# Kernel tuning notes

Hardware: AMD Instinct MI355X
Metric: run time of the kernel (lower is better)

The kernel has to match this reference:

```python
import jax, jax.numpy as jnp
import numpy as np

N_NODES = 10000
N_EDGES = 160000
N_GRAPHS = 64
TOWERS = 5
F_IN = 75        # divide_input=False -> each tower sees full 75-dim input
F_OUT = 15       # 75 // 5 towers
N_LAYERS = 4
POST_IN = (4 * 3 + 1) * F_IN  # (aggregators*scalers + 1) * F_in = 975
AVG_DEG_LOG = float(np.log(17.0))  # avg_deg['log'] from the deg histogram (avg degree 16)
BN_EPS = 1e-5


def setup_inputs() -> dict:
    key = jax.random.key(0)
    ks = jax.random.split(key, 20)
    g = lambda k, shape, s=0.05: (jax.random.normal(k, shape, jnp.float32) * s)
    inp = {}
    inp["x"] = jax.random.normal(ks[0], (N_NODES, 2), jnp.float32)
    inp["edge_index"] = jax.random.randint(ks[1], (2, N_EDGES), 0, N_NODES)
    inp["batch"] = jnp.sort(jax.random.randint(ks[2], (N_NODES,), 0, N_GRAPHS))
    # pre_lin: Linear(2, 75)
    inp["pre_lin_W"] = g(ks[3], (2, 75));   inp["pre_lin_b"] = g(ks[4], (75,))
    # 4 PNAConv layers, params stacked over layers
    inp["pre_W"]  = g(ks[5], (N_LAYERS, TOWERS, 2 * F_IN, F_IN))   # per-tower pre-MLP Linear(150,75)
    inp["pre_b"]  = g(ks[6], (N_LAYERS, TOWERS, F_IN))
    inp["post_W"] = g(ks[7], (N_LAYERS, TOWERS, POST_IN, F_OUT))   # per-tower post-MLP Linear(975,15)
    inp["post_b"] = g(ks[8], (N_LAYERS, TOWERS, F_OUT))
    inp["lin_W"]  = g(ks[9], (N_LAYERS, 75, 75))                    # mixing Linear(75,75)
    inp["lin_b"]  = g(ks[10], (N_LAYERS, 75))
    inp["bn_scale"] = jnp.ones((N_LAYERS, 75), jnp.float32) + g(ks[11], (N_LAYERS, 75))
    inp["bn_bias"]  = g(ks[12], (N_LAYERS, 75))
    # head MLP: 75 -> 50 -> 25 -> 1
    inp["mlp_W1"] = g(ks[13], (75, 50)); inp["mlp_b1"] = g(ks[14], (50,))
    inp["mlp_W2"] = g(ks[15], (50, 25)); inp["mlp_b2"] = g(ks[16], (25,))
    inp["mlp_W3"] = g(ks[17], (25, 1));  inp["mlp_b3"] = g(ks[18], (1,))
    return inp


def _pna_layer(h, src, dst, preW, preb, postW, postb, linW, linb, n):
    # message: concat(x_i, x_j) = concat(x[dst], x[src]), per-tower pre-MLP (pre_layers=1)
    e = jnp.concatenate([h[dst], h[src]], axis=-1)                    # [E, 150]
    m = jnp.einsum('ec,tcf->etf', e, preW) + preb                     # [E, T, 75]
    # multi-aggregate at dst: mean, min, max, std
    cnt = jax.ops.segment_sum(jnp.ones((m.shape[0],), m.dtype), dst, n)  # [N]
    d = jnp.maximum(cnt, 1.0)[:, None, None]                          # clamped degree
    mean = jax.ops.segment_sum(m, dst, n) / d
    mean_sq = jax.ops.segment_sum(m * m, dst, n) / d
    std = jnp.sqrt(jax.nn.relu(mean_sq - mean * mean) + 1e-5)
    empty = (cnt == 0)[:, None, None]
    mn = jnp.where(empty, 0.0, jax.ops.segment_min(m, dst, n))
    mx = jnp.where(empty, 0.0, jax.ops.segment_max(m, dst, n))
    agg = jnp.concatenate([mean, mn, mx, std], axis=-1)               # [N, T, 300]
    # scalers: identity, amplification, attenuation
    logd = jnp.log(d + 1.0)
    out = jnp.concatenate([agg, agg * (logd / AVG_DEG_LOG), agg * (AVG_DEG_LOG / logd)], axis=-1)  # [N, T, 900]
    # concat tower input, per-tower post-MLP, concat towers, final lin
    xt = jnp.broadcast_to(h[:, None, :], (n, TOWERS, F_IN))
    out = jnp.concatenate([xt, out], axis=-1)                         # [N, T, 975]
    out = jnp.einsum('ntc,tcf->ntf', out, postW) + postb              # [N, T, 15]
    out = out.reshape(n, TOWERS * F_OUT)                              # [N, 75]
    return out @ linW + linb


def reference(x, edge_index, batch, pre_lin_W, pre_lin_b, pre_W, pre_b,
              post_W, post_b, lin_W, lin_b, bn_scale, bn_bias,
              mlp_W1, mlp_b1, mlp_W2, mlp_b2, mlp_W3, mlp_b3):
    n = x.shape[0]
    src, dst = edge_index[0], edge_index[1]
    h = x @ pre_lin_W + pre_lin_b
    for l in range(N_LAYERS):
        out = _pna_layer(h, src, dst, pre_W[l], pre_b[l], post_W[l], post_b[l],
                         lin_W[l], lin_b[l], n)
        # BatchNorm1d (training-mode batch stats, biased variance) + ReLU
        mu = out.mean(axis=0)
        var = out.var(axis=0)
        h = jax.nn.relu((out - mu) / jnp.sqrt(var + BN_EPS) * bn_scale[l] + bn_bias[l])
    pooled = jax.ops.segment_sum(h, batch, N_GRAPHS)                  # global_add_pool [G, 75]
    z = jax.nn.relu(pooled @ mlp_W1 + mlp_b1)
    z = jax.nn.relu(z @ mlp_W2 + mlp_b2)
    return z @ mlp_W3 + mlp_b3                                        # [G, 1]
```

## Files before the change

### kernel.cpp

```cpp
#include <hip/hip_runtime.h>

#define NN 10000
#define NE 160000
#define NG 64
#define NT 5
#define NF 75
#define NL 4
#define LOG17 2.8332133f
#define ROWB 384
#define ASTR 328
#define A1STR 104
#define NCT 56

typedef __attribute__((ext_vector_type(8))) short short8v;
typedef __attribute__((ext_vector_type(4))) float float4v;

__device__ __forceinline__ unsigned short f2bf(float x){
  unsigned u = __float_as_uint(x);
  unsigned r = (u + 0x7FFFu + ((u >> 16) & 1u)) >> 16;
  return (unsigned short)r;
}
__device__ __forceinline__ float blo(unsigned u){ return __uint_as_float(u << 16); }
__device__ __forceinline__ float bhi(unsigned u){ return __uint_as_float(u & 0xFFFF0000u); }

__device__ __forceinline__ int swzk(int k){
  int ks = k >> 5, r = k & 31;
  return (ks << 5) | (((r & 15) >> 2) << 3) | ((r >> 4) << 2) | (r & 3);
}
__device__ __forceinline__ short8v ld8(const unsigned short* p){
  union { uint4 u; short8v v; } x;
  x.u = *(const uint4*)p;
  return x.v;
}

__global__ __launch_bounds__(256) void k_init_h(const float* __restrict__ x,
    const float* __restrict__ W, const float* __restrict__ b, float* __restrict__ h){
  int i = blockIdx.x*256 + threadIdx.x;
  if (i >= NN*NF) return;
  int n = i / NF, f = i - n*NF;
  h[i] = x[2*n]*W[f] + x[2*n+1]*W[NF+f] + b[f];
}

__global__ __launch_bounds__(256) void k_count(const int* __restrict__ ei, int* __restrict__ cnt){
  int e = blockIdx.x*256 + threadIdx.x;
  if (e < NE) atomicAdd(&cnt[ei[NE + e]], 1);
}

__global__ __launch_bounds__(1024) void k_scan(const int* __restrict__ cnt,
    int* __restrict__ off, int* __restrict__ cur){
  __shared__ int buf[1024];
  __shared__ int carry;
  int tid = threadIdx.x;
  if (tid == 0) carry = 0;
  __syncthreads();
  for (int base = 0; base < NN; base += 1024){
    int i = base + tid;
    int v = (i < NN) ? cnt[i] : 0;
    buf[tid] = v;
    __syncthreads();
    for (int d = 1; d < 1024; d <<= 1){
      int t = (tid >= d) ? buf[tid - d] : 0;
      __syncthreads();
      buf[tid] += t;
      __syncthreads();
    }
    int c = carry;
    if (i < NN){ int ex = c + buf[tid] - v; off[i] = ex; cur[i] = ex; }
    int tot = buf[1023];
    __syncthreads();
    if (tid == 0) carry = c + tot;
    __syncthreads();
  }
  if (tid == 0) off[NN] = NE;
}

__global__ __launch_bounds__(256) void k_scatter(const int* __restrict__ ei,
    int* __restrict__ cur, int* __restrict__ csr){
  int e = blockIdx.x*256 + threadIdx.x;
  if (e < NE){
    int d = ei[NE + e];
    int p = atomicAdd(&cur[d], 1);
    csr[p] = ei[e];
  }
}

__global__ __launch_bounds__(256) void k_buildWgS(const float* __restrict__ preW,
    const float* __restrict__ postW, unsigned short* __restrict__ WgS){
  const int TOT = NL*NCT*2*16*96;
  int idx = blockIdx.x*256 + threadIdx.x;
  if (idx >= TOT) return;
  int kpos = idx % 96;
  int rem = idx / 96;
  int n = rem & 15; rem >>= 4;
  int p = rem & 1;  rem >>= 1;
  int ct = rem % NCT;
  int l = rem / NCT;
  int ks = kpos >> 5, r = kpos & 31;
  int b = (r >> 3) & 3, half = (r >> 2) & 1, j = r & 3;
  int k = ks*32 + half*16 + b*4 + j;
  int col = ct*16 + n;
  float val = 0.f;
  if (k < 75){
    if (col < 375){
      int t = col/75, f = col - t*75;
      val = preW[((size_t)(l*NT + t)*150 + 75 + k)*75 + f];
    } else if (col >= 384 && col < 759){
      int jj = col - 384; int t = jj/75, f = jj - t*75;
      val = preW[((size_t)(l*NT + t)*150 + k)*75 + f];
    } else if (col >= 768 && col < 843){
      int jj = col - 768; int t = jj/15, f2 = jj - t*15;
      val = postW[((size_t)(l*NT + t)*975 + k)*15 + f2];
    }
  }
  unsigned short hi = f2bf(val);
  unsigned short outv = hi;
  if (p){
    float rsd = val - __uint_as_float(((unsigned)hi) << 16);
    outv = f2bf(rsd);
  }
  WgS[idx] = outv;
}

__global__ __launch_bounds__(256) void k_buildW45S(const float* __restrict__ postW,
    unsigned short* __restrict__ W45S){
  int idx = blockIdx.x*256 + threadIdx.x;
  const int TOT = NL*NT*3*2*16*320;
  if (idx >= TOT) return;
  int kpos = idx % 320;
  int rem = idx / 320;
  int n = rem & 15; rem >>= 4;
  int p = rem & 1;  rem >>= 1;
  int g = rem % 3;  rem /= 3;
  int t = rem % 5;
  int l = rem / 5;
  int ks = kpos >> 5, r = kpos & 31;
  int b = (r >> 3) & 3, half = (r >> 2) & 1, j = r & 3;
  int k = ks*32 + half*16 + b*4 + j;
  float val = 0.f;
  if (n < 15 && k < 300)
    val = postW[((size_t)(l*NT + t)*975 + 75 + g*300 + k)*15 + n];
  unsigned short hi = f2bf(val);
  unsigned short out = hi;
  if (p){
    float rsd = val - __uint_as_float(((unsigned)hi) << 16);
    out = f2bf(rsd);
  }
  W45S[idx] = out;
}

__global__ __launch_bounds__(256) void k_gemm1(const float* __restrict__ src,
    const unsigned short* __restrict__ WgS, const float* __restrict__ preb,
    const float* __restrict__ bnSp, const float* __restrict__ sc,
    const float* __restrict__ bb, int use_bn,
    unsigned short* __restrict__ out1b, float* __restrict__ baseb,
    float* __restrict__ z, int l){
  __shared__ unsigned short Ah[64*A1STR];
  __shared__ unsigned short Al[64*A1STR];
  int tid = threadIdx.x;
  int bid = blockIdx.x;
  int cg = bid / 157, nt = bid - cg*157;
  int n0 = nt*64;

  for (int i = tid; i < 64*A1STR/2; i += 256){
    ((unsigned*)Ah)[i] = 0; ((unsigned*)Al)[i] = 0;
  }
  __syncthreads();
  for (int idx = tid; idx < 64*75; idx += 256){
    int i = idx/75, c = idx - i*75;
    float v = (n0 + i < NN) ? src[(size_t)n0*75 + idx] : 0.f;
    if (use_bn){
      float mu = bnSp[c] * (1.f/NN);
      float var = bnSp[80 + c] * (1.f/NN) - mu*mu;
      v = fmaxf((v - mu) / sqrtf(var + 1e-5f) * sc[c] + bb[c], 0.f);
    }
    unsigned short hi = f2bf(v);
    float rsd = v - __uint_as_float(((unsigned)hi) << 16);
    int p = i*A1STR + swzk(c);
    Ah[p] = hi; Al[p] = f2bf(rsd);
  }
  __syncthreads();

  int w = tid >> 6, lane = tid & 63;
  int bq = lane >> 4, low = lane & 15;
  const unsigned short* ah = &Ah[(w*16 + low)*A1STR];
  const unsigned short* al = &Al[(w*16 + low)*A1STR];

  float4v acc[8];
  #pragma unroll
  for (int ct = 0; ct < 8; ++ct) acc[ct] = (float4v){0.f,0.f,0.f,0.f};

  #pragma unroll
  for (int ks = 0; ks < 3; ++ks){
    int o = ks*32 + bq*8;
    short8v a_h = ld8(ah + o);
    short8v a_l = ld8(al + o);
    #pragma unroll
    for (int ct = 0; ct < 8; ++ct){
      int gct = cg*8 + ct;
      const unsigned short* wbase = WgS + (((size_t)l*NCT + gct)*2)*16*96 + low*96 + o;
      short8v b_h = ld8(wbase);
      short8v b_l = ld8(wbase + 16*96);
      acc[ct] = __builtin_amdgcn_mfma_f32_16x16x32_bf16(a_h, b_h, acc[ct], 0, 0, 0);
      acc[ct] = __builtin_amdgcn_mfma_f32_16x16x32_bf16(a_h, b_l, acc[ct], 0, 0, 0);
      acc[ct] = __builtin_amdgcn_mfma_f32_16x16x32_bf16(a_l, b_h, acc[ct], 0, 0, 0);
    }
  }

  #pragma unroll
  for (int ct = 0; ct < 8; ++ct){
    int col = cg*128 + ct*16 + low;
    #pragma unroll
    for (int i = 0; i < 4; ++i){
      int n = n0 + w*16 + bq*4 + i;
      if (n < NN){
        float v = acc[ct][i];
        if (col < 375){
          out1b[(size_t)n*ROWB + col] = f2bf(v);
        } else if (col >= 384 && col < 759){
          baseb[(size_t)n*376 + (col - 384)] = v + preb[l*375 + (col - 384)];
        } else if (col >= 768 && col < 843){
          z[(size_t)n*75 + (col - 768)] = v;
        }
      }
    }
  }
}

__device__ __forceinline__ uint4 pack8(const float* v){
  uint4 r;
  r.x = (unsigned)f2bf(v[0]) | ((unsigned)f2bf(v[1]) << 16);
  r.y = (unsigned)f2bf(v[2]) | ((unsigned)f2bf(v[3]) << 16);
  r.z = (unsigned)f2bf(v[4]) | ((unsigned)f2bf(v[5]) << 16);
  r.w = (unsigned)f2bf(v[6]) | ((unsigned)f2bf(v[7]) << 16);
  return r;
}

__global__ __launch_bounds__(256) void k_gather(
    const unsigned short* __restrict__ out1b, const float* __restrict__ baseb,
    const int* __restrict__ off, const int* __restrict__ csr,
    unsigned short* __restrict__ agg){
  int gid = blockIdx.x*256 + threadIdx.x;
  int n = gid >> 6;
  int lane = gid & 63;
  if (n >= NN || lane >= 47) return;
  int fo = lane*8;
  float s[8], ss[8], mn[8], mx[8];
  #pragma unroll
  for (int j = 0; j < 8; ++j){ s[j]=0.f; ss[j]=0.f; mn[j]=3.4e38f; mx[j]=-3.4e38f; }
  int e0 = off[n], e1 = off[n+1], deg = e1 - e0;

#define STT(v,J){ float _v=(v); s[J]+=_v; ss[J]+=_v*_v; mn[J]=fminf(mn[J],_v); mx[J]=fmaxf(mx[J],_v); }
#define PR(X){ STT(blo((X).x),0) STT(bhi((X).x),1) STT(blo((X).y),2) STT(bhi((X).y),3) \
               STT(blo((X).z),4) STT(bhi((X).z),5) STT(blo((X).w),6) STT(bhi((X).w),7) }
  int k = e0;
  for (; k + 4 <= e1; k += 4){
    uint4 a  = *(const uint4*)(out1b + (size_t)csr[k]  *ROWB + fo);
    uint4 b  = *(const uint4*)(out1b + (size_t)csr[k+1]*ROWB + fo);
    uint4 c  = *(const uint4*)(out1b + (size_t)csr[k+2]*ROWB + fo);
    uint4 d2 = *(const uint4*)(out1b + (size_t)csr[k+3]*ROWB + fo);
    PR(a) PR(b) PR(c) PR(d2)
  }
  for (; k < e1; ++k){
    uint4 a = *(const uint4*)(out1b + (size_t)csr[k]*ROWB + fo);
    PR(a)
  }
#undef PR
#undef STT

  float mean[8], sd[8];
  if (deg > 0){
    float rd = 1.f/(float)deg;
    float4 b0 = *(const float4*)(baseb + (size_t)n*376 + fo);
    float4 b1 = *(const float4*)(baseb + (size_t)n*376 + fo + 4);
    float bs[8] = {b0.x,b0.y,b0.z,b0.w,b1.x,b1.y,b1.z,b1.w};
    #pragma unroll
    for (int j = 0; j < 8; ++j){
      float mb = s[j]*rd;
      float var = ss[j]*rd - mb*mb;
      mean[j] = bs[j] + mb;
      sd[j]   = sqrtf(fmaxf(var, 0.f) + 1e-5f);
      mn[j]   = bs[j] + mn[j];
      mx[j]   = bs[j] + mx[j];
    }
  } else {
    #pragma unroll
    for (int j = 0; j < 8; ++j){ mean[j]=0.f; mn[j]=0.f; mx[j]=0.f; sd[j]=sqrtf(1e-5f); }
  }
  unsigned short* ap = agg + (size_t)n*1504 + fo;
  *(uint4*)(ap)        = pack8(mean);
  *(uint4*)(ap + 376)  = pack8(mn);
  *(uint4*)(ap + 752)  = pack8(mx);
  *(uint4*)(ap + 1128) = pack8(sd);
}

__global__ __launch_bounds__(128) void k_post(
    const unsigned short* __restrict__ agg, float* __restrict__ z,
    const int* __restrict__ off, const unsigned short* __restrict__ W45S,
    const float* __restrict__ postb, int l){
  __shared__ unsigned short As[32*ASTR];
  __shared__ float ampl[32], attl[32];
  int tid = threadIdx.x;
  int bid = blockIdx.x;
  const int NTILE = (NN + 31)/32;
  int t = bid / NTILE, nt = bid - t*NTILE;
  int n0 = nt*32;
  if (tid < 32){
    int n = n0 + tid;
    int dd = (n < NN) ? (off[n+1] - off[n]) : 1;
    float d = (float)(dd > 0 ? dd : 1);
    float logd = logf(d + 1.f);
    ampl[tid] = logd*(1.f/LOG17);
    attl[tid] = LOG17/logd;
  }
  for (int idx = tid; idx < 32*320; idx += 128){
    int nl = idx/320, c = idx - nl*320;
    int n = n0 + nl;
    unsigned short raw = 0;
    if (n < NN && c < 300){
      int st = c/75, u = c - st*75;
      raw = agg[(size_t)n*1504 + st*376 + t*75 + u];
    }
    As[nl*ASTR + swzk(c)] = raw;
  }
  __syncthreads();

  int w = tid >> 6, lane = tid & 63;
  int bq = lane >> 4, low = lane & 15;
  const unsigned short* ab = &As[(w*16 + low)*ASTR];
  const unsigned short* wb = W45S + (size_t)((l*NT + t)*3)*2*16*320;
  const unsigned short* b0h = wb + (size_t)(0*2+0)*16*320 + low*320;
  const unsigned short* b0l = wb + (size_t)(0*2+1)*16*320 + low*320;
  const unsigned short* b1h = wb + (size_t)(1*2+0)*16*320 + low*320;
  const unsigned short* b1l = wb + (size_t)(1*2+1)*16*320 + low*320;
  const unsigned short* b2h = wb + (size_t)(2*2+0)*16*320 + low*320;
  const unsigned short* b2l = wb + (size_t)(2*2+1)*16*320 + low*320;

  float4v acc0 = {0.f,0.f,0.f,0.f};
  float4v acc1 = {0.f,0.f,0.f,0.f};
  float4v acc2 = {0.f,0.f,0.f,0.f};
  for (int ks = 0; ks < 10; ++ks){
    int o = ks*32 + bq*8;
    short8v a = ld8(ab + o);
    acc0 = __builtin_amdgcn_mfma_f32_16x16x32_bf16(a, ld8(b0h + o), acc0, 0, 0, 0);
    acc1 = __builtin_amdgcn_mfma_f32_16x16x32_bf16(a, ld8(b1h + o), acc1, 0, 0, 0);
    acc2 = __builtin_amdgcn_mfma_f32_16x16x32_bf16(a, ld8(b2h + o), acc2, 0, 0, 0);
    acc0 = __builtin_amdgcn_mfma_f32_16x16x32_bf16(a, ld8(b0l + o), acc0, 0, 0, 0);
    acc1 = __builtin_amdgcn_mfma_f32_16x16x32_bf16(a, ld8(b1l + o), acc1, 0, 0, 0);
    acc2 = __builtin_amdgcn_mfma_f32_16x16x32_bf16(a, ld8(b2l + o), acc2, 0, 0, 0);
  }

  if (low < 15){
    float pb = postb[(l*NT + t)*15 + low];
    #pragma unroll
    for (int i = 0; i < 4; ++i){
      int m = bq*4 + i;
      int node = n0 + w*16 + m;
      if (node < NN){
        float val = acc0[i] + ampl[w*16 + m]*acc1[i] + attl[w*16 + m]*acc2[i] + pb;
        z[(size_t)node*75 + t*15 + low] += val;
      }
    }
  }
}

__global__ __launch_bounds__(256) void k_lin(const float* __restrict__ z,
    const float* __restrict__ linW, const float* __restrict__ linb,
    float* __restrict__ out2, float* __restrict__ bnS1, int l){
  __shared__ float zs[75][68];
  __shared__ float lw[75][80];
  int tid = threadIdx.x;
  int n0 = blockIdx.x*64;
  for (int idx = tid; idx < 64*75; idx += 256){
    int i = idx/75, c = idx - i*75;
    zs[c][i] = (n0 + i < NN) ? z[(size_t)n0*75 + idx] : 0.f;
  }
  for (int idx = tid; idx < 75*80; idx += 256){
    int c = idx/80, o = idx - c*80;
    lw[c][o] = (o < 75) ? linW[(size_t)l*5625 + c*75 + o] : 0.f;
  }
  __syncthreads();
  int og = tid >> 4, n4 = tid & 15;
  int o0 = og*5;
  float acc[4][5];
  #pragma unroll
  for (int i = 0; i < 4; ++i)
    #pragma unroll
    for (int k = 0; k < 5; ++k) acc[i][k] = 0.f;
  for (int c = 0; c < 75; ++c){
    float4 a = *reinterpret_cast<const float4*>(&zs[c][n4*4]);
    float av[4] = {a.x, a.y, a.z, a.w};
    float wv[5];
    #pragma unroll
    for (int k = 0; k < 5; ++k) wv[k] = lw[c][o0 + k];
    #pragma unroll
    for (int i = 0; i < 4; ++i)
      #pragma unroll
      for (int k = 0; k < 5; ++k) acc[i][k] += av[i]*wv[k];
  }
  float s1p[5], s2p[5];
  #pragma unroll
  for (int k = 0; k < 5; ++k){ s1p[k] = 0.f; s2p[k] = 0.f; }
  #pragma unroll
  for (int i = 0; i < 4; ++i){
    int n = n0 + n4*4 + i;
    if (n >= NN) continue;
    #pragma unroll
    for (int k = 0; k < 5; ++k){
      int o = o0 + k;
      if (o < 75){
        float v = acc[i][k] + linb[l*75 + o];
        out2[(size_t)n*75 + o] = v;
        s1p[k] += v; s2p[k] += v*v;
      }
    }
  }
  __syncthreads();
  float* red = &zs[0][0];
  #pragma unroll
  for (int k = 0; k < 5; ++k){
    int o = o0 + k;
    if (o < 75){ red[o*16 + n4] = s1p[k]; red[1200 + o*16 + n4] = s2p[k]; }
  }
  __syncthreads();
  if (tid < 75){
    float a1 = 0.f, a2 = 0.f;
    #pragma unroll
    for (int j = 0; j < 16; ++j){ a1 += red[tid*16 + j]; a2 += red[1200 + tid*16 + j]; }
    atomicAdd(&bnS1[tid], a1);
    atomicAdd(&bnS1[80 + tid], a2);
  }
}

__global__ __launch_bounds__(256) void k_bnpool(const float* __restrict__ out2,
    const float* __restrict__ bnSp, const float* __restrict__ sc,
    const float* __restrict__ bb, const int* __restrict__ batch,
    float* __restrict__ pooled){
  int i = blockIdx.x*256 + threadIdx.x;
  if (i >= NN*75) return;
  int n = i / 75, f = i - n*75;
  float mu = bnSp[f] * (1.f/NN);
  float var = bnSp[80 + f] * (1.f/NN) - mu*mu;
  float v = fmaxf((out2[i] - mu) / sqrtf(var + 1e-5f) * sc[f] + bb[f], 0.f);
  atomicAdd(&pooled[batch[n]*75 + f], v);
}

__global__ __launch_bounds__(256) void k_head(const float* __restrict__ pooled,
    const float* __restrict__ W1, const float* __restrict__ b1,
    const float* __restrict__ W2, const float* __restrict__ b2,
    const float* __restrict__ W3, const float* __restrict__ b3,
    float* __restrict__ out){
  __shared__ float pl[64*75];
  __shared__ float w1[75*50];
  __shared__ float z1[64*50];
  __shared__ float w2[50*25];
  __shared__ float z2[64*25];
  __shared__ float w3[25];
  __shared__ float bb1[50], bb2[25];
  int tid = threadIdx.x;
  for (int i = tid; i < 64*75; i += 256) pl[i] = pooled[i];
  for (int i = tid; i < 75*50; i += 256) w1[i] = W1[i];
  for (int i = tid; i < 50*25; i += 256) w2[i] = W2[i];
  if (tid < 25) w3[tid] = W3[tid];
  if (tid < 50) bb1[tid] = b1[tid];
  if (tid < 25) bb2[tid] = b2[tid];
  __syncthreads();
  for (int o = tid; o < 64*50; o += 256){
    int g = o / 50, j = o - g*50;
    float acc = bb1[j];
    for (int c = 0; c < 75; ++c) acc += pl[g*75 + c] * w1[c*50 + j];
    z1[o] = fmaxf(acc, 0.f);
  }
  __syncthreads();
  for (int o = tid; o < 64*25; o += 256){
    int g = o / 25, j = o - g*25;
    float acc = bb2[j];
    for (int c = 0; c < 50; ++c) acc += z1[g*50 + c] * w2[c*25 + j];
    z2[o] = fmaxf(acc, 0.f);
  }
  __syncthreads();
  if (tid < 64){
    float acc = b3[0];
    for (int c = 0; c < 25; ++c) acc += z2[tid*25 + c] * w3[c];
    out[tid] = acc;
  }
}

extern "C" void kernel_launch(void* const* d_in, const int* in_sizes, int n_in,
                              void* d_out, int out_size, void* d_ws, size_t ws_size,
                              hipStream_t stream){
  const float* x     = (const float*)d_in[0];
  const int*   ei    = (const int*)  d_in[1];
  const int*   batch = (const int*)  d_in[2];
  const float* plW   = (const float*)d_in[3];
  const float* plb   = (const float*)d_in[4];
  const float* preW  = (const float*)d_in[5];
  const float* preb  = (const float*)d_in[6];
  const float* postW = (const float*)d_in[7];
  const float* postb = (const float*)d_in[8];
  const float* linW  = (const float*)d_in[9];
  const float* linb  = (const float*)d_in[10];
  const float* bns   = (const float*)d_in[11];
  const float* bnb   = (const float*)d_in[12];
  const float* W1    = (const float*)d_in[13];
  const float* b1    = (const float*)d_in[14];
  const float* W2    = (const float*)d_in[15];
  const float* b2    = (const float*)d_in[16];
  const float* W3    = (const float*)d_in[17];
  const float* b3    = (const float*)d_in[18];
  float* out = (float*)d_out;

  float* out2v = (float*)d_ws;
  float* zv    = out2v + 750000;
  float* baseb = zv + 750000;
  unsigned short* W45S = (unsigned short*)(baseb + (size_t)NN*376);
  unsigned short* WgS  = W45S + (size_t)NL*NT*3*2*16*320;
  float* pooled= (float*)(WgS + (size_t)NL*NCT*2*16*96);
  float* bnS   = pooled + 4800;
  unsigned short* out1b = (unsigned short*)(bnS + NL*160);
  unsigned short* aggb  = out1b + (size_t)NN*ROWB;
  float* h0 = (float*)(aggb + (size_t)NN*1504) - 750000;
  int* cnt = (int*)(aggb + (size_t)NN*1504);
  int* off = cnt + NN;
  int* cur = off + NN + 1;
  int* csr = cur + NN;

  hipMemsetAsync(cnt, 0, NN*sizeof(int), stream);
  hipMemsetAsync(bnS, 0, NL*160*sizeof(float), stream);
  hipMemsetAsync(pooled, 0, 4800*sizeof(float), stream);
  hipMemsetAsync(out1b, 0, (size_t)NN*ROWB*sizeof(unsigned short), stream);
  k_init_h<<<(NN*NF + 255)/256, 256, 0, stream>>>(x, plW, plb, h0);
  k_count<<<(NE + 255)/256, 256, 0, stream>>>(ei, cnt);
  k_scan<<<1, 1024, 0, stream>>>(cnt, off, cur);
  k_scatter<<<(NE + 255)/256, 256, 0, stream>>>(ei, cur, csr);
  k_buildWgS<<<(NL*NCT*2*16*96 + 255)/256, 256, 0, stream>>>(preW, postW, WgS);
  k_buildW45S<<<(NL*NT*3*2*16*320 + 255)/256, 256, 0, stream>>>(postW, W45S);

  const int NTILE = (NN + 31)/32;

  for (int l = 0; l < NL; ++l){
    const float* src = (l == 0) ? h0 : out2v;
    const float* bnSp = bnS + (l > 0 ? (l-1)*160 : 0);
    const float* sc = bns + (l > 0 ? (l-1)*75 : 0);
    const float* bb = bnb + (l > 0 ? (l-1)*75 : 0);
    k_gemm1<<<7*157, 256, 0, stream>>>(src, WgS, preb, bnSp, sc, bb, (l > 0),
                                       out1b, baseb, zv, l);
    k_gather<<<(NN*64)/256, 256, 0, stream>>>(out1b, baseb, off, csr, aggb);
    k_post<<<NT*NTILE, 128, 0, stream>>>(aggb, zv, off, W45S, postb, l);
    k_lin<<<157, 256, 0, stream>>>(zv, linW, linb, out2v, bnS + l*160, l);
  }

  k_bnpool<<<(NN*NF + 255)/256, 256, 0, stream>>>(out2v, bnS + 3*160,
                                                  bns + 3*75, bnb + 3*75, batch, pooled);
  k_head<<<1, 256, 0, stream>>>(pooled, W1, b1, W2, b2, W3, b3, out);
}
```

Measured before the change: 655.7 us.

## Pad per-tower features to 80 and write MFMA-swizzled aggregates directly

Rows of out1b and baseb are re-laid out so each tower's 75 features sit in an 80-wide padded slot. The gather kernel now writes the mean/min/max/std aggregates straight into the swizzled per-tower K layout that the post GEMM consumes. This lets k_post load A fragments directly from global memory instead of staging them through shared memory with scalar gathers. The cost is slightly more padded memory and gather threads, and the post weights are rebuilt to match the padded K indexing.

```diff
diff --git a/kernel.cpp b/kernel.cpp
--- a/kernel.cpp
+++ b/kernel.cpp
@@ -7,8 +7,7 @@
 #define NF 75
 #define NL 4
 #define LOG17 2.8332133f
-#define ROWB 384
-#define ASTR 328
+#define ROWP 400
 #define A1STR 104
 #define NCT 56
 
@@ -135,10 +134,11 @@
   int l = rem / 5;
   int ks = kpos >> 5, r = kpos & 31;
   int b = (r >> 3) & 3, half = (r >> 2) & 1, j = r & 3;
-  int k = ks*32 + half*16 + b*4 + j;
+  int kp = ks*32 + half*16 + b*4 + j;
+  int stat = kp / 80, u = kp - stat*80;
   float val = 0.f;
-  if (n < 15 && k < 300)
-    val = postW[((size_t)(l*NT + t)*975 + 75 + g*300 + k)*15 + n];
+  if (n < 15 && u < 75)
+    val = postW[((size_t)(l*NT + t)*975 + 75 + g*300 + stat*75 + u)*15 + n];
   unsigned short hi = f2bf(val);
   unsigned short out = hi;
   if (p){
@@ -215,9 +215,11 @@
       if (n < NN){
         float v = acc[ct][i];
         if (col < 375){
-          out1b[(size_t)n*ROWB + col] = f2bf(v);
+          int t = col/75, u = col - t*75;
+          out1b[(size_t)n*ROWP + t*80 + u] = f2bf(v);
         } else if (col >= 384 && col < 759){
-          baseb[(size_t)n*376 + (col - 384)] = v + preb[l*375 + (col - 384)];
+          int f = col - 384; int t = f/75, u = f - t*75;
+          baseb[(size_t)n*ROWP + t*80 + u] = v + preb[l*375 + f];
         } else if (col >= 768 && col < 843){
           z[(size_t)n*75 + (col - 768)] = v;
         }
@@ -226,12 +228,10 @@
   }
 }
 
-__device__ __forceinline__ uint4 pack8(const float* v){
-  uint4 r;
+__device__ __forceinline__ uint2 pack4(const float* v){
+  uint2 r;
   r.x = (unsigned)f2bf(v[0]) | ((unsigned)f2bf(v[1]) << 16);
   r.y = (unsigned)f2bf(v[2]) | ((unsigned)f2bf(v[3]) << 16);
-  r.z = (unsigned)f2bf(v[4]) | ((unsigned)f2bf(v[5]) << 16);
-  r.w = (unsigned)f2bf(v[6]) | ((unsigned)f2bf(v[7]) << 16);
   return r;
 }
 
@@ -242,8 +242,9 @@
   int gid = blockIdx.x*256 + threadIdx.x;
   int n = gid >> 6;
   int lane = gid & 63;
-  if (n >= NN || lane >= 47) return;
-  int fo = lane*8;
+  if (n >= NN || lane >= 50) return;
+  int p = lane*8;
+  int t = p/80, u0 = p - t*80;
   float s[8], ss[8], mn[8], mx[8];
   #pragma unroll
   for (int j = 0; j < 8; ++j){ s[j]=0.f; ss[j]=0.f; mn[j]=3.4e38f; mx[j]=-3.4e38f; }
@@ -254,14 +255,14 @@
                STT(blo((X).z),4) STT(bhi((X).z),5) STT(blo((X).w),6) STT(bhi((X).w),7) }
   int k = e0;
   for (; k + 4 <= e1; k += 4){
-    uint4 a  = *(const uint4*)(out1b + (size_t)csr[k]  *ROWB + fo);
-    uint4 b  = *(const uint4*)(out1b + (size_t)csr[k+1]*ROWB + fo);
-    uint4 c  = *(const uint4*)(out1b + (size_t)csr[k+2]*ROWB + fo);
-    uint4 d2 = *(const uint4*)(out1b + (size_t)csr[k+3]*ROWB + fo);
+    uint4 a  = *(const uint4*)(out1b + (size_t)csr[k]  *ROWP + p);
+    uint4 b  = *(const uint4*)(out1b + (size_t)csr[k+1]*ROWP + p);
+    uint4 c  = *(const uint4*)(out1b + (size_t)csr[k+2]*ROWP + p);
+    uint4 d2 = *(const uint4*)(out1b + (size_t)csr[k+3]*ROWP + p);
     PR(a) PR(b) PR(c) PR(d2)
   }
   for (; k < e1; ++k){
-    uint4 a = *(const uint4*)(out1b + (size_t)csr[k]*ROWB + fo);
+    uint4 a = *(const uint4*)(out1b + (size_t)csr[k]*ROWP + p);
     PR(a)
   }
 #undef PR
@@ -270,8 +271,8 @@
   float mean[8], sd[8];
   if (deg > 0){
     float rd = 1.f/(float)deg;
-    float4 b0 = *(const float4*)(baseb + (size_t)n*376 + fo);
-    float4 b1 = *(const float4*)(baseb + (size_t)n*376 + fo + 4);
+    float4 b0 = *(const float4*)(baseb + (size_t)n*ROWP + p);
+    float4 b1 = *(const float4*)(baseb + (size_t)n*ROWP + p + 4);
     float bs[8] = {b0.x,b0.y,b0.z,b0.w,b1.x,b1.y,b1.z,b1.w};
     #pragma unroll
     for (int j = 0; j < 8; ++j){
@@ -286,18 +287,25 @@
     #pragma unroll
     for (int j = 0; j < 8; ++j){ mean[j]=0.f; mn[j]=0.f; mx[j]=0.f; sd[j]=sqrtf(1e-5f); }
   }
-  unsigned short* ap = agg + (size_t)n*1504 + fo;
-  *(uint4*)(ap)        = pack8(mean);
-  *(uint4*)(ap + 376)  = pack8(mn);
-  *(uint4*)(ap + 752)  = pack8(mx);
-  *(uint4*)(ap + 1128) = pack8(sd);
+  #pragma unroll
+  for (int j = 0; j < 8; ++j){
+    if (u0 + j >= 75){ mean[j]=0.f; mn[j]=0.f; mx[j]=0.f; sd[j]=0.f; }
+  }
+  unsigned short* ap = agg + (size_t)n*1600 + t*320;
+  *(uint2*)(ap + swzk(0*80 + u0))     = pack4(mean);
+  *(uint2*)(ap + swzk(0*80 + u0 + 4)) = pack4(mean + 4);
+  *(uint2*)(ap + swzk(1*80 + u0))     = pack4(mn);
+  *(uint2*)(ap + swzk(1*80 + u0 + 4)) = pack4(mn + 4);
+  *(uint2*)(ap + swzk(2*80 + u0))     = pack4(mx);
+  *(uint2*)(ap + swzk(2*80 + u0 + 4)) = pack4(mx + 4);
+  *(uint2*)(ap + swzk(3*80 + u0))     = pack4(sd);
+  *(uint2*)(ap + swzk(3*80 + u0 + 4)) = pack4(sd + 4);
 }
 
 __global__ __launch_bounds__(128) void k_post(
     const unsigned short* __restrict__ agg, float* __restrict__ z,
     const int* __restrict__ off, const unsigned short* __restrict__ W45S,
     const float* __restrict__ postb, int l){
-  __shared__ unsigned short As[32*ASTR];
   __shared__ float ampl[32], attl[32];
   int tid = threadIdx.x;
   int bid = blockIdx.x;
@@ -312,21 +320,13 @@
     ampl[tid] = logd*(1.f/LOG17);
     attl[tid] = LOG17/logd;
   }
-  for (int idx = tid; idx < 32*320; idx += 128){
-    int nl = idx/320, c = idx - nl*320;
-    int n = n0 + nl;
-    unsigned short raw = 0;
-    if (n < NN && c < 300){
-      int st = c/75, u = c - st*75;
-      raw = agg[(size_t)n*1504 + st*376 + t*75 + u];
-    }
-    As[nl*ASTR + swzk(c)] = raw;
-  }
   __syncthreads();
 
   int w = tid >> 6, lane = tid & 63;
   int bq = lane >> 4, low = lane & 15;
-  const unsigned short* ab = &As[(w*16 + low)*ASTR];
+  int node = n0 + w*16 + low;
+  int ncl = (node < NN) ? node : (NN - 1);
+  const unsigned short* ab = agg + (size_t)ncl*1600 + t*320;
   const unsigned short* wb = W45S + (size_t)((l*NT + t)*3)*2*16*320;
   const unsigned short* b0h = wb + (size_t)(0*2+0)*16*320 + low*320;
   const unsigned short* b0l = wb + (size_t)(0*2+1)*16*320 + low*320;
@@ -338,6 +338,7 @@
   float4v acc0 = {0.f,0.f,0.f,0.f};
   float4v acc1 = {0.f,0.f,0.f,0.f};
   float4v acc2 = {0.f,0.f,0.f,0.f};
+  #pragma unroll
   for (int ks = 0; ks < 10; ++ks){
     int o = ks*32 + bq*8;
     short8v a = ld8(ab + o);
@@ -354,10 +355,10 @@
     #pragma unroll
     for (int i = 0; i < 4; ++i){
       int m = bq*4 + i;
-      int node = n0 + w*16 + m;
-      if (node < NN){
+      int nd = n0 + w*16 + m;
+      if (nd < NN){
         float val = acc0[i] + ampl[w*16 + m]*acc1[i] + attl[w*16 + m]*acc2[i] + pb;
-        z[(size_t)node*75 + t*15 + low] += val;
+        z[(size_t)nd*75 + t*15 + low] += val;
       }
     }
   }
@@ -512,14 +513,14 @@
   float* out2v = (float*)d_ws;
   float* zv    = out2v + 750000;
   float* baseb = zv + 750000;
-  unsigned short* W45S = (unsigned short*)(baseb + (size_t)NN*376);
+  unsigned short* W45S = (unsigned short*)(baseb + (size_t)NN*ROWP);
   unsigned short* WgS  = W45S + (size_t)NL*NT*3*2*16*320;
   float* pooled= (float*)(WgS + (size_t)NL*NCT*2*16*96);
   float* bnS   = pooled + 4800;
   unsigned short* out1b = (unsigned short*)(bnS + NL*160);
-  unsigned short* aggb  = out1b + (size_t)NN*ROWB;
-  float* h0 = (float*)(aggb + (size_t)NN*1504) - 750000;
-  int* cnt = (int*)(aggb + (size_t)NN*1504);
+  unsigned short* aggb  = out1b + (size_t)NN*ROWP;
+  float* h0 = (float*)(aggb + (size_t)NN*1600) - 750000;
+  int* cnt = (int*)(aggb + (size_t)NN*1600);
   int* off = cnt + NN;
   int* cur = off + NN + 1;
   int* csr = cur + NN;
@@ -527,7 +528,7 @@
   hipMemsetAsync(cnt, 0, NN*sizeof(int), stream);
   hipMemsetAsync(bnS, 0, NL*160*sizeof(float), stream);
   hipMemsetAsync(pooled, 0, 4800*sizeof(float), stream);
-  hipMemsetAsync(out1b, 0, (size_t)NN*ROWB*sizeof(unsigned short), stream);
+  hipMemsetAsync(out1b, 0, (size_t)NN*ROWP*sizeof(unsigned short), stream);
   k_init_h<<<(NN*NF + 255)/256, 256, 0, stream>>>(x, plW, plb, h0);
   k_count<<<(NE + 255)/256, 256, 0, stream>>>(ei, cnt);
   k_scan<<<1, 1024, 0, stream>>>(cnt, off, cur);
```

Result: faster. 570.3 us (-13.0%).
